# Performance work log

Hardware: AMD Instinct MI355X
Metric: run time of the kernel (lower is better)

## Reference

```python
import jax, jax.numpy as jnp
import numpy as np

N, E, D, L = 100000, 600000, 128, 5
EPS = 1e-5


def setup_inputs() -> dict:
    key = jax.random.key(0)
    ks = jax.random.split(key, 32)
    ri = lambda k, shape, hi: jax.random.randint(k, shape, 0, hi)
    rn = lambda k, shape: jax.random.normal(k, shape, jnp.float32) * 0.02
    inp = {
        'atomic_num': ri(ks[0], (N,), 119),
        'formal_charge': ri(ks[1], (N,), 11),
        'chiral_tag': ri(ks[2], (N,), 5),
        'hybridization': ri(ks[3], (N,), 8),
        'num_explicit_hs': ri(ks[4], (N,), 6),
        'is_aromatic': ri(ks[5], (N,), 2),
        'edge_index': ri(ks[6], (2, E), N),
        'is_conjugated': ri(ks[7], (E,), 2),
        'edge_is_aromatic': ri(ks[8], (E,), 2),
        'bond_type': ri(ks[9], (E,), 22),
        'bond_dir': ri(ks[10], (E,), 7),
        'bond_stereo': ri(ks[11], (E,), 6),
        # atom embedding tables (vocab sizes are typical RDKit cardinalities)
        'emb_atomic_num': rn(ks[12], (120, D)),
        'emb_formal_charge': rn(ks[13], (12, D)),
        'emb_chiral_tag': rn(ks[14], (5, D)),
        'emb_hybridization': rn(ks[15], (8, D)),
        'emb_num_explicit_hs': rn(ks[16], (6, D)),
        'emb_is_aromatic': rn(ks[17], (2, D)),
        # per-layer edge embedding tables, stacked on leading layer axis
        'e_conj': rn(ks[18], (L, 3, D)),
        'e_arom': rn(ks[19], (L, 3, D)),
        'e_btype': rn(ks[20], (L, 23, D)),
        'e_bdir': rn(ks[21], (L, 8, D)),
        'e_bstereo': rn(ks[22], (L, 7, D)),
        # per-layer GIN MLP (D -> 2D -> D)
        'mlp_w1': rn(ks[23], (L, D, 2 * D)),
        'mlp_b1': jnp.zeros((L, 2 * D), jnp.float32),
        'mlp_w2': rn(ks[24], (L, 2 * D, D)),
        'mlp_b2': jnp.zeros((L, D), jnp.float32),
        # per-layer batchnorm affine params (training-mode batch stats)
        'bn_gamma': jnp.ones((L, D), jnp.float32),
        'bn_beta': jnp.zeros((L, D), jnp.float32),
    }
    return inp


def reference(atomic_num, formal_charge, chiral_tag, hybridization,
              num_explicit_hs, is_aromatic, edge_index,
              is_conjugated, edge_is_aromatic, bond_type, bond_dir, bond_stereo,
              emb_atomic_num, emb_formal_charge, emb_chiral_tag,
              emb_hybridization, emb_num_explicit_hs, emb_is_aromatic,
              e_conj, e_arom, e_btype, e_bdir, e_bstereo,
              mlp_w1, mlp_b1, mlp_w2, mlp_b2, bn_gamma, bn_beta):
    # seed node features: sum of atom-feature embeddings  [N, D]
    h = (emb_atomic_num[atomic_num] + emb_formal_charge[formal_charge]
         + emb_chiral_tag[chiral_tag] + emb_hybridization[hybridization]
         + emb_num_explicit_hs[num_explicit_hs] + emb_is_aromatic[is_aromatic])
    src, dst = edge_index[0], edge_index[1]
    for l in range(L):
        # edge embeddings: sum of bond-feature embeddings  [E, D]
        eemb = (e_conj[l][is_conjugated] + e_arom[l][edge_is_aromatic]
                + e_btype[l][bond_type] + e_bdir[l][bond_dir]
                + e_bstereo[l][bond_stereo])
        # self-loop edges use bond-feature index 0 for every feature  [D]
        self_vec = e_conj[l, 0] + e_arom[l, 0] + e_btype[l, 0] + e_bdir[l, 0] + e_bstereo[l, 0]
        # GIN message: x_j + edge_attr, scatter-add at dst; self loops folded in analytically
        msg = h[src] + eemb                                      # [E, D]
        agg = jax.ops.segment_sum(msg, dst, num_segments=N) + h + self_vec
        # GIN update MLP: D -> 2D -> D
        hid = jax.nn.relu(agg @ mlp_w1[l] + mlp_b1[l])
        h = hid @ mlp_w2[l] + mlp_b2[l]
        # batch norm over the node dimension (training-mode batch statistics)
        mean = h.mean(axis=0)
        var = h.var(axis=0)
        h = bn_gamma[l] * (h - mean) * jax.lax.rsqrt(var + EPS) + bn_beta[l]
        if l < L - 1:
            h = jax.nn.relu(h)
        # dropout_ratio = 0.0 -> identity
    return h  # JK='last', graph_pooling=None -> node representations [N, D]
```

## Files before the change

### kernel.cpp

```cpp
#include <hip/hip_runtime.h>

#define NN 100000
#define EE 600000
#define DD 128
#define LL 5
#define CTROWS 5152
#define MBLK 1563
#define TILES 1563
#define PBLK 256
#define SBLK 98

typedef float f32x4 __attribute__((ext_vector_type(4)));
typedef _Float16 f16x8 __attribute__((ext_vector_type(8)));
typedef _Float16 f16x4 __attribute__((ext_vector_type(4)));

__global__ __launch_bounds__(256) void seed_kernel(
    const int* __restrict__ an, const int* __restrict__ fc,
    const int* __restrict__ ct, const int* __restrict__ hy,
    const int* __restrict__ nh, const int* __restrict__ ar,
    const float* __restrict__ ean, const float* __restrict__ efc,
    const float* __restrict__ ect, const float* __restrict__ ehy,
    const float* __restrict__ enh, const float* __restrict__ ear,
    _Float16* __restrict__ h)
{
    int idx = blockIdx.x * 256 + threadIdx.x;
    int n = idx >> 4, q = idx & 15;
    f32x4 a0 = ((const f32x4*)(ean + an[n] * DD))[2 * q];
    f32x4 a1 = ((const f32x4*)(ean + an[n] * DD))[2 * q + 1];
    a0 += ((const f32x4*)(efc + fc[n] * DD))[2 * q];
    a1 += ((const f32x4*)(efc + fc[n] * DD))[2 * q + 1];
    a0 += ((const f32x4*)(ect + ct[n] * DD))[2 * q];
    a1 += ((const f32x4*)(ect + ct[n] * DD))[2 * q + 1];
    a0 += ((const f32x4*)(ehy + hy[n] * DD))[2 * q];
    a1 += ((const f32x4*)(ehy + hy[n] * DD))[2 * q + 1];
    a0 += ((const f32x4*)(enh + nh[n] * DD))[2 * q];
    a1 += ((const f32x4*)(enh + nh[n] * DD))[2 * q + 1];
    a0 += ((const f32x4*)(ear + ar[n] * DD))[2 * q];
    a1 += ((const f32x4*)(ear + ar[n] * DD))[2 * q + 1];
    f16x8 o;
    #pragma unroll
    for (int j = 0; j < 4; ++j) { o[j] = (_Float16)a0[j]; o[j + 4] = (_Float16)a1[j]; }
    ((f16x8*)h)[idx] = o;
}

__global__ __launch_bounds__(256) void convw1_kernel(const float* __restrict__ w1,
                                                     _Float16* __restrict__ w1t)
{
    int idx = blockIdx.x * 256 + threadIdx.x;
    int l = idx >> 15, rem = idx & 32767;
    int n = rem >> 7, k = rem & 127;
    w1t[idx] = (_Float16)w1[l * 32768 + k * 256 + n];
}
__global__ __launch_bounds__(256) void convw2_kernel(const float* __restrict__ w2,
                                                     _Float16* __restrict__ w2t)
{
    int idx = blockIdx.x * 256 + threadIdx.x;
    int l = idx >> 15, rem = idx & 32767;
    int n = rem >> 8, k = rem & 255;
    w2t[idx] = (_Float16)w2[l * 32768 + k * 128 + n];
}

__global__ void idss_kernel(float* __restrict__ idss)
{
    int t = threadIdx.x;
    idss[t] = (t < 128) ? 1.0f : 0.0f;
}

__global__ __launch_bounds__(256) void count_kernel(const int* __restrict__ ei,
                                                    int* __restrict__ cursor)
{
    int e = blockIdx.x * 256 + threadIdx.x;
    if (e < EE) atomicAdd(&cursor[ei[EE + e]], 1);
}

__global__ __launch_bounds__(1024) void btot_kernel(const int* __restrict__ cursor,
                                                    int* __restrict__ btot)
{
    __shared__ int wsum[16];
    int tid = threadIdx.x;
    int i = blockIdx.x * 1024 + tid;
    int x = (i < NN) ? cursor[i] : 0;
    #pragma unroll
    for (int off = 1; off < 64; off <<= 1) x += __shfl_xor(x, off, 64);
    if ((tid & 63) == 0) wsum[tid >> 6] = x;
    __syncthreads();
    if (tid == 0) {
        int s = 0;
        #pragma unroll
        for (int w = 0; w < 16; ++w) s += wsum[w];
        btot[blockIdx.x] = s;
    }
}

__global__ __launch_bounds__(128) void bscan_kernel(const int* __restrict__ btot,
                                                    int* __restrict__ boff,
                                                    int* __restrict__ rowstart)
{
    __shared__ int w0;
    int t = threadIdx.x;
    int lane = t & 63, wv = t >> 6;
    int x = (t < SBLK) ? btot[t] : 0;
    int incl = x;
    #pragma unroll
    for (int off = 1; off < 64; off <<= 1) {
        int u = __shfl_up(incl, off, 64);
        if (lane >= off) incl += u;
    }
    if (wv == 0 && lane == 63) w0 = incl;
    __syncthreads();
    if (wv == 1) incl += w0;
    if (t < SBLK) boff[t] = incl - x;
    if (t == 127) rowstart[NN] = incl;
}

__global__ __launch_bounds__(1024) void apply_kernel(const int* __restrict__ cursorin,
                                                     const int* __restrict__ boff,
                                                     int* __restrict__ rowstart,
                                                     int* __restrict__ cursor)
{
    __shared__ int wsum[16];
    int tid = threadIdx.x;
    int lane = tid & 63, wv = tid >> 6;
    int i = blockIdx.x * 1024 + tid;
    int x = (i < NN) ? cursorin[i] : 0;
    int incl = x;
    #pragma unroll
    for (int off = 1; off < 64; off <<= 1) {
        int u = __shfl_up(incl, off, 64);
        if (lane >= off) incl += u;
    }
    if (lane == 63) wsum[wv] = incl;
    __syncthreads();
    int pre = 0;
    #pragma unroll
    for (int w = 0; w < 16; ++w) pre += (w < wv) ? wsum[w] : 0;
    int excl = boff[blockIdx.x] + pre + incl - x;
    if (i < NN) { rowstart[i] = excl; cursor[i] = excl; }
}

__global__ __launch_bounds__(256) void fill_kernel(
    const int* __restrict__ ei, int* __restrict__ cursor, int* __restrict__ rec,
    const int* __restrict__ f0, const int* __restrict__ f1,
    const int* __restrict__ f2, const int* __restrict__ f3,
    const int* __restrict__ f4)
{
    int e = blockIdx.x * 256 + threadIdx.x;
    if (e >= EE) return;
    int dst = ei[EE + e];
    int p = atomicAdd(&cursor[dst], 1);
    int f = f0[e] + 2 * (f1[e] + 2 * (f2[e] + 23 * (f3[e] + 8 * f4[e])));
    rec[p] = ei[e] | (f << 17);
}

__global__ __launch_bounds__(256) void ctab_kernel(
    const float* __restrict__ ec, const float* __restrict__ ea,
    const float* __restrict__ eb, const float* __restrict__ ed,
    const float* __restrict__ es, _Float16* __restrict__ ctab)
{
    int idx = blockIdx.x * 256 + threadIdx.x;
    int row = idx >> 4, q = idx & 15;
    int conj = row & 1, arom = (row >> 1) & 1;
    int r2 = row >> 2;
    int bt = r2 % 23, r3 = r2 / 23;
    int bd = r3 & 7, bs = r3 >> 3;
    f32x4 a0 = ((const f32x4*)(ec + conj * DD))[2 * q]
             + ((const f32x4*)(ea + arom * DD))[2 * q]
             + ((const f32x4*)(eb + bt * DD))[2 * q]
             + ((const f32x4*)(ed + bd * DD))[2 * q]
             + ((const f32x4*)(es + bs * DD))[2 * q];
    f32x4 a1 = ((const f32x4*)(ec + conj * DD))[2 * q + 1]
             + ((const f32x4*)(ea + arom * DD))[2 * q + 1]
             + ((const f32x4*)(eb + bt * DD))[2 * q + 1]
             + ((const f32x4*)(ed + bd * DD))[2 * q + 1]
             + ((const f32x4*)(es + bs * DD))[2 * q + 1];
    f16x8 o;
    #pragma unroll
    for (int j = 0; j < 4; ++j) { o[j] = (_Float16)a0[j]; o[j + 4] = (_Float16)a1[j]; }
    ((f16x8*)ctab)[idx] = o;
}

__global__ __launch_bounds__(256) void gather_bn_kernel(
    const _Float16* __restrict__ hsrc, _Float16* __restrict__ agg,
    const int* __restrict__ rowstart, const int* __restrict__ rec,
    const _Float16* __restrict__ ctab, const float* __restrict__ ss, int dorelu)
{
    int idx = blockIdx.x * 256 + threadIdx.x;
    int n = idx >> 4, q = idx & 15;
    f32x4 sc0 = ((const f32x4*)ss)[2 * q],        sc1 = ((const f32x4*)ss)[2 * q + 1];
    f32x4 sh0 = ((const f32x4*)(ss + 128))[2 * q], sh1 = ((const f32x4*)(ss + 128))[2 * q + 1];
    int p0 = rowstart[n], p1 = rowstart[n + 1];
    f16x8 x = ((const f16x8*)hsrc)[idx];
    f16x8 c0 = ((const f16x8*)ctab)[q];
    float v[8];
    #pragma unroll
    for (int j = 0; j < 8; ++j) {
        float sc = (j < 4) ? sc0[j] : sc1[j - 4];
        float sh = (j < 4) ? sh0[j] : sh1[j - 4];
        float t = (float)x[j] * sc + sh;
        if (dorelu && t < 0.f) t = 0.f;
        v[j] = t + (float)c0[j];
    }
    if (p0 < p1) {
        int r0 = rec[p0];
        int r1 = (p0 + 1 < p1) ? rec[p0 + 1] : r0;
        f16x8 y0 = *(const f16x8*)(hsrc + (size_t)(r0 & 0x1FFFF) * DD + q * 8);
        f16x8 e0 = *(const f16x8*)(ctab + (size_t)(((unsigned)r0) >> 17) * DD + q * 8);
        for (int p = p0; p < p1; ++p) {
            int r2 = (p + 2 < p1) ? rec[p + 2] : r1;
            f16x8 y1 = *(const f16x8*)(hsrc + (size_t)(r1 & 0x1FFFF) * DD + q * 8);
            f16x8 e1 = *(const f16x8*)(ctab + (size_t)(((unsigned)r1) >> 17) * DD + q * 8);
            #pragma unroll
            for (int j = 0; j < 8; ++j) {
                float sc = (j < 4) ? sc0[j] : sc1[j - 4];
                float sh = (j < 4) ? sh0[j] : sh1[j - 4];
                float t = (float)y0[j] * sc + sh;
                if (dorelu && t < 0.f) t = 0.f;
                v[j] += t + (float)e0[j];
            }
            y0 = y1; e0 = e1; r1 = r2;
        }
    }
    f16x8 o;
    #pragma unroll
    for (int j = 0; j < 8; ++j) o[j] = (_Float16)v[j];
    ((f16x8*)agg)[idx] = o;
}

__global__ __launch_bounds__(256, 1) void mlp_kernel(
    const _Float16* __restrict__ A, const _Float16* __restrict__ w1t,
    const _Float16* __restrict__ w2t,
    const float* __restrict__ b1, const float* __restrict__ b2,
    _Float16* __restrict__ hpre, float* __restrict__ psum, float* __restrict__ psq,
    int M)
{
    __shared__ _Float16 hid[8 * 4 * 64 * 8];
    int tid = threadIdx.x;
    int w = tid >> 6, lane = tid & 63;
    int ln = lane & 15, quad = lane >> 4;
    const f32x4 zero = {0.f, 0.f, 0.f, 0.f};

    int t0 = (blockIdx.x * TILES) >> 8;
    int t1 = ((blockIdx.x + 1) * TILES) >> 8;

    f16x8 ba[4][4];
    #pragma unroll
    for (int ns = 0; ns < 4; ++ns) {
        int row = t0 * 64 + ns * 16 + ln;
        row = row < M ? row : M - 1;
        #pragma unroll
        for (int kt = 0; kt < 4; ++kt)
            ba[ns][kt] = *(const f16x8*)(A + (size_t)row * 128 + kt * 32 + quad * 8);
    }

    f16x8 w1f[4][4];
    #pragma unroll
    for (int n1 = 0; n1 < 4; ++n1)
        #pragma unroll
        for (int kt = 0; kt < 4; ++kt)
            w1f[n1][kt] = *(const f16x8*)(w1t + (w * 64 + n1 * 16 + ln) * 128 + kt * 32 + quad * 8);
    f32x4 b1v[4];
    #pragma unroll
    for (int n1 = 0; n1 < 4; ++n1)
        b1v[n1] = *(const f32x4*)(b1 + w * 64 + n1 * 16 + quad * 4);

    f16x8 w2f[2][8];
    #pragma unroll
    for (int n2 = 0; n2 < 2; ++n2)
        #pragma unroll
        for (int kt2 = 0; kt2 < 8; ++kt2)
            w2f[n2][kt2] = *(const f16x8*)(w2t + (w * 32 + n2 * 16 + ln) * 256 + kt2 * 32 + quad * 8);
    f32x4 b2v[2];
    #pragma unroll
    for (int n2 = 0; n2 < 2; ++n2)
        b2v[n2] = *(const f32x4*)(b2 + w * 32 + n2 * 16 + quad * 4);

    f32x4 ssum[2] = {zero, zero};
    f32x4 sqsum[2] = {zero, zero};

    for (int t = t0; t < t1; ++t) {
        int node0 = t * 64;

        #pragma unroll
        for (int ns = 0; ns < 4; ++ns) {
            f32x4 acc1[4] = {zero, zero, zero, zero};
            #pragma unroll
            for (int kt = 0; kt < 4; ++kt)
                #pragma unroll
                for (int n1 = 0; n1 < 4; ++n1)
                    acc1[n1] = __builtin_amdgcn_mfma_f32_16x16x32_f16(w1f[n1][kt], ba[ns][kt], acc1[n1], 0, 0, 0);
            {
                int row = (t + 1) * 64 + ns * 16 + ln;
                row = row < M ? row : M - 1;
                #pragma unroll
                for (int kt = 0; kt < 4; ++kt)
                    ba[ns][kt] = *(const f16x8*)(A + (size_t)row * 128 + kt * 32 + quad * 8);
            }
            #pragma unroll
            for (int n1 = 0; n1 < 4; ++n1) {
                int a = w * 4 + n1;
                f16x4 pk;
                #pragma unroll
                for (int r = 0; r < 4; ++r) {
                    float v = acc1[n1][r] + b1v[n1][r];
                    v = v > 0.f ? v : 0.f;
                    pk[r] = (_Float16)v;
                }
                int lp = ((a & 1) * 2 + (quad >> 1)) * 16 + ln;
                int off = (((a >> 1) * 4 + ns) * 64 + lp) * 8 + (quad & 1) * 4;
                *(f16x4*)(&hid[off]) = pk;
            }
        }

        __syncthreads();

        #pragma unroll
        for (int ns = 0; ns < 4; ++ns) {
            f32x4 acc2[2] = {zero, zero};
            #pragma unroll
            for (int kt2 = 0; kt2 < 8; ++kt2) {
                f16x8 bf = *(const f16x8*)(&hid[((kt2 * 4 + ns) * 64 + lane) * 8]);
                acc2[0] = __builtin_amdgcn_mfma_f32_16x16x32_f16(w2f[0][kt2], bf, acc2[0], 0, 0, 0);
                acc2[1] = __builtin_amdgcn_mfma_f32_16x16x32_f16(w2f[1][kt2], bf, acc2[1], 0, 0, 0);
            }
            int node = node0 + ns * 16 + ln;
            bool valid = node < M;
            #pragma unroll
            for (int n2 = 0; n2 < 2; ++n2) {
                f32x4 v;
                f16x4 pk;
                #pragma unroll
                for (int r = 0; r < 4; ++r) {
                    v[r] = acc2[n2][r] + b2v[n2][r];
                    pk[r] = (_Float16)v[r];
                }
                if (valid) {
                    *(f16x4*)(hpre + (size_t)node * 128 + w * 32 + n2 * 16 + quad * 4) = pk;
                    ssum[n2] += v;
                    sqsum[n2] += v * v;
                }
            }
        }

        __syncthreads();
    }

    #pragma unroll
    for (int n2 = 0; n2 < 2; ++n2)
        #pragma unroll
        for (int off = 1; off < 16; off <<= 1)
            #pragma unroll
            for (int r = 0; r < 4; ++r) {
                ssum[n2][r] += __shfl_xor(ssum[n2][r], off, 64);
                sqsum[n2][r] += __shfl_xor(sqsum[n2][r], off, 64);
            }
    if (ln == 0) {
        #pragma unroll
        for (int n2 = 0; n2 < 2; ++n2) {
            *(f32x4*)(psum + blockIdx.x * 128 + w * 32 + n2 * 16 + quad * 4) = ssum[n2];
            *(f32x4*)(psq + blockIdx.x * 128 + w * 32 + n2 * 16 + quad * 4) = sqsum[n2];
        }
    }
}

__global__ __launch_bounds__(256) void reduce_kernel(
    const float* __restrict__ psum, const float* __restrict__ psq,
    const float* __restrict__ gamma, const float* __restrict__ beta,
    float* __restrict__ ss, int nblk)
{
    int c = blockIdx.x;
    int tid = threadIdx.x;
    float s = 0.f, q = 0.f;
    for (int b = tid; b < nblk; b += 256) {
        s += psum[b * 128 + c];
        q += psq[b * 128 + c];
    }
    #pragma unroll
    for (int off = 1; off < 64; off <<= 1) {
        s += __shfl_xor(s, off, 64);
        q += __shfl_xor(q, off, 64);
    }
    __shared__ float rs[4], rq[4];
    int wave = tid >> 6;
    if ((tid & 63) == 0) { rs[wave] = s; rq[wave] = q; }
    __syncthreads();
    if (tid == 0) {
        s = rs[0] + rs[1] + rs[2] + rs[3];
        q = rq[0] + rq[1] + rq[2] + rq[3];
        const float invN = 1.0f / NN;
        float mean = s * invN;
        float var = q * invN - mean * mean;
        float inv = rsqrtf(var + 1e-5f);
        float scale = gamma[c] * inv;
        ss[c] = scale;
        ss[128 + c] = beta[c] - mean * scale;
    }
}

__global__ __launch_bounds__(256) void final_bn_kernel(
    const _Float16* __restrict__ hpre, float* __restrict__ out,
    const float* __restrict__ ss)
{
    int idx = blockIdx.x * 256 + threadIdx.x;
    int q = idx & 15;
    f16x8 x = ((const f16x8*)hpre)[idx];
    f32x4 sc0 = ((const f32x4*)ss)[2 * q],        sc1 = ((const f32x4*)ss)[2 * q + 1];
    f32x4 sh0 = ((const f32x4*)(ss + 128))[2 * q], sh1 = ((const f32x4*)(ss + 128))[2 * q + 1];
    f32x4 y0, y1;
    #pragma unroll
    for (int j = 0; j < 4; ++j) {
        y0[j] = (float)x[j] * sc0[j] + sh0[j];
        y1[j] = (float)x[j + 4] * sc1[j] + sh1[j];
    }
    ((f32x4*)out)[2 * idx] = y0;
    ((f32x4*)out)[2 * idx + 1] = y1;
}

extern "C" void kernel_launch(void* const* d_in, const int* in_sizes, int n_in,
                              void* d_out, int out_size, void* d_ws, size_t ws_size,
                              hipStream_t stream)
{
    const int* an  = (const int*)d_in[0];
    const int* fc  = (const int*)d_in[1];
    const int* ct  = (const int*)d_in[2];
    const int* hy  = (const int*)d_in[3];
    const int* nh  = (const int*)d_in[4];
    const int* ar  = (const int*)d_in[5];
    const int* ei  = (const int*)d_in[6];
    const int* econ = (const int*)d_in[7];
    const int* earo = (const int*)d_in[8];
    const int* ebt  = (const int*)d_in[9];
    const int* ebd  = (const int*)d_in[10];
    const int* ebs  = (const int*)d_in[11];
    const float* ean = (const float*)d_in[12];
    const float* efc = (const float*)d_in[13];
    const float* ect = (const float*)d_in[14];
    const float* ehy = (const float*)d_in[15];
    const float* enh = (const float*)d_in[16];
    const float* ear = (const float*)d_in[17];
    const float* e_conj   = (const float*)d_in[18];
    const float* e_arom   = (const float*)d_in[19];
    const float* e_btype  = (const float*)d_in[20];
    const float* e_bdir   = (const float*)d_in[21];
    const float* e_bstereo= (const float*)d_in[22];
    const float* mlp_w1 = (const float*)d_in[23];
    const float* mlp_b1 = (const float*)d_in[24];
    const float* mlp_w2 = (const float*)d_in[25];
    const float* mlp_b2 = (const float*)d_in[26];
    const float* bn_gamma = (const float*)d_in[27];
    const float* bn_beta  = (const float*)d_in[28];

    _Float16* h0   = (_Float16*)d_ws;
    _Float16* agg  = h0 + (size_t)NN * DD;
    _Float16* hpre = agg + (size_t)NN * DD;
    _Float16* w1t  = hpre + (size_t)NN * DD;
    _Float16* w2t  = w1t + LL * 256 * 128;
    _Float16* ctab = w2t + LL * 128 * 256;
    float*    psum = (float*)(ctab + CTROWS * DD);
    float*    psq  = psum + MBLK * 128;
    float*    ss   = psq + MBLK * 128;
    float*    idss = ss + 256;
    int* rowstart = (int*)(idss + 256);
    int* cursor   = rowstart + NN + 8;
    int* rec      = cursor + NN;
    int* btot     = rec + EE;
    int* boff     = btot + SBLK + 8;

    convw1_kernel<<<640, 256, 0, stream>>>(mlp_w1, w1t);
    convw2_kernel<<<640, 256, 0, stream>>>(mlp_w2, w2t);
    seed_kernel<<<6250, 256, 0, stream>>>(an, fc, ct, hy, nh, ar,
                                          ean, efc, ect, ehy, enh, ear, h0);
    idss_kernel<<<1, 256, 0, stream>>>(idss);

    hipMemsetAsync(cursor, 0, NN * sizeof(int), stream);
    count_kernel<<<2344, 256, 0, stream>>>(ei, cursor);
    btot_kernel<<<SBLK, 1024, 0, stream>>>(cursor, btot);
    bscan_kernel<<<1, 128, 0, stream>>>(btot, boff, rowstart);
    apply_kernel<<<SBLK, 1024, 0, stream>>>(cursor, boff, rowstart, cursor);
    fill_kernel<<<2344, 256, 0, stream>>>(ei, cursor, rec,
                                          econ, earo, ebt, ebd, ebs);

    for (int l = 0; l < LL; ++l) {
        ctab_kernel<<<322, 256, 0, stream>>>(
            e_conj + l * 3 * DD, e_arom + l * 3 * DD, e_btype + l * 23 * DD,
            e_bdir + l * 8 * DD, e_bstereo + l * 7 * DD, ctab);
        gather_bn_kernel<<<6250, 256, 0, stream>>>(
            (l == 0) ? h0 : hpre, agg, rowstart, rec, ctab,
            (l == 0) ? idss : ss, (l == 0) ? 0 : 1);
        mlp_kernel<<<PBLK, 256, 0, stream>>>(
            agg, w1t + l * 32768, w2t + l * 32768,
            mlp_b1 + l * 256, mlp_b2 + l * 128,
            hpre, psum, psq, NN);
        reduce_kernel<<<128, 256, 0, stream>>>(
            psum, psq, bn_gamma + l * 128, bn_beta + l * 128, ss, PBLK);
    }
    final_bn_kernel<<<6250, 256, 0, stream>>>(hpre, (float*)d_out, ss);
}
```

Baseline: 586.1 us.

## Batch edge tables, use packed fp16 gather math, double-buffer MLP LDS

The per-layer edge-combination tables for all five layers are now built in a single launch before the layer loop, removing one kernel launch per layer. The gather kernel does the batchnorm scale, shift and ReLU in packed fp16 vector math, using a -60000 clamp to stand in for no ReLU. It also prefetches neighbor rows and edge embeddings three deep instead of two. The MLP kernel double-buffers its shared hidden tile so the trailing per-tile __syncthreads can be dropped. The fp16 normalization trades some precision for fewer conversions and ALU instructions.

```diff
diff --git a/kernel.cpp b/kernel.cpp
--- a/kernel.cpp
+++ b/kernel.cpp
@@ -155,28 +155,35 @@
 __global__ __launch_bounds__(256) void ctab_kernel(
     const float* __restrict__ ec, const float* __restrict__ ea,
     const float* __restrict__ eb, const float* __restrict__ ed,
-    const float* __restrict__ es, _Float16* __restrict__ ctab)
+    const float* __restrict__ es, _Float16* __restrict__ ctab5)
 {
     int idx = blockIdx.x * 256 + threadIdx.x;
-    int row = idx >> 4, q = idx & 15;
+    int q = idx & 15;
+    int grow = idx >> 4;
+    int l = grow / CTROWS, row = grow - l * CTROWS;
     int conj = row & 1, arom = (row >> 1) & 1;
     int r2 = row >> 2;
     int bt = r2 % 23, r3 = r2 / 23;
     int bd = r3 & 7, bs = r3 >> 3;
-    f32x4 a0 = ((const f32x4*)(ec + conj * DD))[2 * q]
-             + ((const f32x4*)(ea + arom * DD))[2 * q]
-             + ((const f32x4*)(eb + bt * DD))[2 * q]
-             + ((const f32x4*)(ed + bd * DD))[2 * q]
-             + ((const f32x4*)(es + bs * DD))[2 * q];
-    f32x4 a1 = ((const f32x4*)(ec + conj * DD))[2 * q + 1]
-             + ((const f32x4*)(ea + arom * DD))[2 * q + 1]
-             + ((const f32x4*)(eb + bt * DD))[2 * q + 1]
-             + ((const f32x4*)(ed + bd * DD))[2 * q + 1]
-             + ((const f32x4*)(es + bs * DD))[2 * q + 1];
+    const float* ecl = ec + l * 3 * DD;
+    const float* eal = ea + l * 3 * DD;
+    const float* ebl = eb + l * 23 * DD;
+    const float* edl = ed + l * 8 * DD;
+    const float* esl = es + l * 7 * DD;
+    f32x4 a0 = ((const f32x4*)(ecl + conj * DD))[2 * q]
+             + ((const f32x4*)(eal + arom * DD))[2 * q]
+             + ((const f32x4*)(ebl + bt * DD))[2 * q]
+             + ((const f32x4*)(edl + bd * DD))[2 * q]
+             + ((const f32x4*)(esl + bs * DD))[2 * q];
+    f32x4 a1 = ((const f32x4*)(ecl + conj * DD))[2 * q + 1]
+             + ((const f32x4*)(eal + arom * DD))[2 * q + 1]
+             + ((const f32x4*)(ebl + bt * DD))[2 * q + 1]
+             + ((const f32x4*)(edl + bd * DD))[2 * q + 1]
+             + ((const f32x4*)(esl + bs * DD))[2 * q + 1];
     f16x8 o;
     #pragma unroll
     for (int j = 0; j < 4; ++j) { o[j] = (_Float16)a0[j]; o[j + 4] = (_Float16)a1[j]; }
-    ((f16x8*)ctab)[idx] = o;
+    ((f16x8*)ctab5)[idx] = o;
 }
 
 __global__ __launch_bounds__(256) void gather_bn_kernel(
@@ -186,38 +193,39 @@
 {
     int idx = blockIdx.x * 256 + threadIdx.x;
     int n = idx >> 4, q = idx & 15;
-    f32x4 sc0 = ((const f32x4*)ss)[2 * q],        sc1 = ((const f32x4*)ss)[2 * q + 1];
-    f32x4 sh0 = ((const f32x4*)(ss + 128))[2 * q], sh1 = ((const f32x4*)(ss + 128))[2 * q + 1];
+    f16x8 sc8, sh8, clampv;
+    _Float16 cl = dorelu ? (_Float16)0.0f : (_Float16)(-60000.0f);
+    #pragma unroll
+    for (int j = 0; j < 8; ++j) {
+        sc8[j] = (_Float16)ss[q * 8 + j];
+        sh8[j] = (_Float16)ss[128 + q * 8 + j];
+        clampv[j] = cl;
+    }
     int p0 = rowstart[n], p1 = rowstart[n + 1];
     f16x8 x = ((const f16x8*)hsrc)[idx];
     f16x8 c0 = ((const f16x8*)ctab)[q];
+    f16x8 ts = __builtin_elementwise_max((f16x8)(x * sc8 + sh8), clampv);
     float v[8];
     #pragma unroll
-    for (int j = 0; j < 8; ++j) {
-        float sc = (j < 4) ? sc0[j] : sc1[j - 4];
-        float sh = (j < 4) ? sh0[j] : sh1[j - 4];
-        float t = (float)x[j] * sc + sh;
-        if (dorelu && t < 0.f) t = 0.f;
-        v[j] = t + (float)c0[j];
-    }
+    for (int j = 0; j < 8; ++j) v[j] = (float)ts[j] + (float)c0[j];
+
     if (p0 < p1) {
         int r0 = rec[p0];
         int r1 = (p0 + 1 < p1) ? rec[p0 + 1] : r0;
+        int rr2 = (p0 + 2 < p1) ? rec[p0 + 2] : r1;
         f16x8 y0 = *(const f16x8*)(hsrc + (size_t)(r0 & 0x1FFFF) * DD + q * 8);
         f16x8 e0 = *(const f16x8*)(ctab + (size_t)(((unsigned)r0) >> 17) * DD + q * 8);
+        f16x8 y1 = *(const f16x8*)(hsrc + (size_t)(r1 & 0x1FFFF) * DD + q * 8);
+        f16x8 e1 = *(const f16x8*)(ctab + (size_t)(((unsigned)r1) >> 17) * DD + q * 8);
         for (int p = p0; p < p1; ++p) {
-            int r2 = (p + 2 < p1) ? rec[p + 2] : r1;
-            f16x8 y1 = *(const f16x8*)(hsrc + (size_t)(r1 & 0x1FFFF) * DD + q * 8);
-            f16x8 e1 = *(const f16x8*)(ctab + (size_t)(((unsigned)r1) >> 17) * DD + q * 8);
+            int r3 = (p + 3 < p1) ? rec[p + 3] : rr2;
+            f16x8 y2 = *(const f16x8*)(hsrc + (size_t)(rr2 & 0x1FFFF) * DD + q * 8);
+            f16x8 e2 = *(const f16x8*)(ctab + (size_t)(((unsigned)rr2) >> 17) * DD + q * 8);
+            f16x8 t = __builtin_elementwise_max((f16x8)(y0 * sc8 + sh8), clampv);
+            f16x8 u = t + e0;
             #pragma unroll
-            for (int j = 0; j < 8; ++j) {
-                float sc = (j < 4) ? sc0[j] : sc1[j - 4];
-                float sh = (j < 4) ? sh0[j] : sh1[j - 4];
-                float t = (float)y0[j] * sc + sh;
-                if (dorelu && t < 0.f) t = 0.f;
-                v[j] += t + (float)e0[j];
-            }
-            y0 = y1; e0 = e1; r1 = r2;
+            for (int j = 0; j < 8; ++j) v[j] += (float)u[j];
+            y0 = y1; e0 = e1; y1 = y2; e1 = e2; rr2 = r3;
         }
     }
     f16x8 o;
@@ -233,7 +241,7 @@
     _Float16* __restrict__ hpre, float* __restrict__ psum, float* __restrict__ psq,
     int M)
 {
-    __shared__ _Float16 hid[8 * 4 * 64 * 8];
+    __shared__ _Float16 hid[2][8 * 4 * 64 * 8];
     int tid = threadIdx.x;
     int w = tid >> 6, lane = tid & 63;
     int ln = lane & 15, quad = lane >> 4;
@@ -279,6 +287,7 @@
 
     for (int t = t0; t < t1; ++t) {
         int node0 = t * 64;
+        _Float16* hb = hid[t & 1];
 
         #pragma unroll
         for (int ns = 0; ns < 4; ++ns) {
@@ -307,7 +316,7 @@
                 }
                 int lp = ((a & 1) * 2 + (quad >> 1)) * 16 + ln;
                 int off = (((a >> 1) * 4 + ns) * 64 + lp) * 8 + (quad & 1) * 4;
-                *(f16x4*)(&hid[off]) = pk;
+                *(f16x4*)(hb + off) = pk;
             }
         }
 
@@ -318,7 +327,7 @@
             f32x4 acc2[2] = {zero, zero};
             #pragma unroll
             for (int kt2 = 0; kt2 < 8; ++kt2) {
-                f16x8 bf = *(const f16x8*)(&hid[((kt2 * 4 + ns) * 64 + lane) * 8]);
+                f16x8 bf = *(const f16x8*)(hb + ((kt2 * 4 + ns) * 64 + lane) * 8);
                 acc2[0] = __builtin_amdgcn_mfma_f32_16x16x32_f16(w2f[0][kt2], bf, acc2[0], 0, 0, 0);
                 acc2[1] = __builtin_amdgcn_mfma_f32_16x16x32_f16(w2f[1][kt2], bf, acc2[1], 0, 0, 0);
             }
@@ -340,8 +349,6 @@
                 }
             }
         }
-
-        __syncthreads();
     }
 
     #pragma unroll
@@ -454,8 +461,8 @@
     _Float16* hpre = agg + (size_t)NN * DD;
     _Float16* w1t  = hpre + (size_t)NN * DD;
     _Float16* w2t  = w1t + LL * 256 * 128;
-    _Float16* ctab = w2t + LL * 128 * 256;
-    float*    psum = (float*)(ctab + CTROWS * DD);
+    _Float16* ctab5= w2t + LL * 128 * 256;
+    float*    psum = (float*)(ctab5 + (size_t)LL * CTROWS * DD);
     float*    psq  = psum + MBLK * 128;
     float*    ss   = psq + MBLK * 128;
     float*    idss = ss + 256;
@@ -470,6 +477,8 @@
     seed_kernel<<<6250, 256, 0, stream>>>(an, fc, ct, hy, nh, ar,
                                           ean, efc, ect, ehy, enh, ear, h0);
     idss_kernel<<<1, 256, 0, stream>>>(idss);
+    ctab_kernel<<<1610, 256, 0, stream>>>(e_conj, e_arom, e_btype,
+                                          e_bdir, e_bstereo, ctab5);
 
     hipMemsetAsync(cursor, 0, NN * sizeof(int), stream);
     count_kernel<<<2344, 256, 0, stream>>>(ei, cursor);
@@ -480,11 +489,9 @@
                                           econ, earo, ebt, ebd, ebs);
 
     for (int l = 0; l < LL; ++l) {
-        ctab_kernel<<<322, 256, 0, stream>>>(
-            e_conj + l * 3 * DD, e_arom + l * 3 * DD, e_btype + l * 23 * DD,
-            e_bdir + l * 8 * DD, e_bstereo + l * 7 * DD, ctab);
         gather_bn_kernel<<<6250, 256, 0, stream>>>(
-            (l == 0) ? h0 : hpre, agg, rowstart, rec, ctab,
+            (l == 0) ? h0 : hpre, agg, rowstart, rec,
+            ctab5 + (size_t)l * CTROWS * DD,
             (l == 0) ? idss : ss, (l == 0) ? 0 : 1);
         mlp_kernel<<<PBLK, 256, 0, stream>>>(
             agg, w1t + l * 32768, w2t + l * 32768,
```

Result: faster. 570.9 us (-2.6%).
